# Kernel optimization log

Hardware: AMD Instinct MI355X
Metric: run time of the kernel (lower is better)

Reference implementation:

```python
import jax, jax.numpy as jnp
import numpy as np

WS = 10
NUM_HEADS = 12
DIM = 384


def setup_inputs() -> dict:
    key = jax.random.key(0)
    k1, k2, k3 = jax.random.split(key, 3)
    B, t, H, W, C = 2, 4, 44, 44, DIM
    x = jax.random.normal(k1, (B * t, H * W, C), dtype=jnp.float32)
    qkv_w = jax.random.normal(k2, (3 * C, C), dtype=jnp.float32) * 0.02
    proj_w = jax.random.normal(k3, (C, C), dtype=jnp.float32) * 0.02
    proj_b = jnp.zeros((C,), dtype=jnp.float32)
    return {"x": x, "qkv_w": qkv_w, "proj_w": proj_w, "proj_b": proj_b,
            "t": t, "H": H, "W": W}


def reference(x, qkv_w, proj_w, proj_b, t, H, W):
    ws, nh = WS, NUM_HEADS
    BT, N, C = x.shape
    B = BT // t
    hd = C // nh
    scale = hd ** (-0.5)

    ax = x.reshape(B, t, H, W, C)
    pad_r = (ws - W % ws) % ws
    pad_b = (ws - H % ws) % ws
    if pad_r > 0 or pad_b > 0:
        ax = jnp.pad(ax, ((0, 0), (0, 0), (0, pad_b), (0, pad_r), (0, 0)))
    hg, wg = (H + ws - 1) // ws, (W + ws - 1) // ws
    # partition into windows: each window holds t*ws*ws tokens
    ax = ax.reshape(B, t, hg, ws, wg, ws, C)
    ax = ax.transpose(0, 2, 4, 1, 3, 5, 6).reshape(B, hg * wg, t * ws * ws, C)

    qkv = ax @ qkv_w.T  # (B, nw, n, 3C)
    qkv = qkv.reshape(B, hg * wg, t * ws * ws, 3, nh, hd)
    qkv = qkv.transpose(3, 0, 1, 4, 2, 5)  # (3, B, nw, nh, n, hd)
    q, k, v = qkv[0], qkv[1], qkv[2]

    attn = jnp.einsum('bwhnd,bwhmd->bwhnm', q, k) * scale
    attn = jax.nn.softmax(attn, axis=-1)
    out = jnp.einsum('bwhnm,bwhmd->bwhnd', attn, v)  # (B, nw, nh, n, hd)
    out = out.transpose(0, 1, 3, 2, 4).reshape(B, hg * wg, t * ws * ws, C)

    # reverse window partition
    out = out.reshape(B, hg, wg, t, ws, ws, C)
    out = out.transpose(0, 3, 1, 4, 2, 5, 6).reshape(B, t, hg * ws, wg * ws, C)
    out = out[:, :, :H, :W, :]
    out = out.reshape(B, t * H * W, C)
    out = out @ proj_w.T + proj_b
    return out.reshape(-1, N, C)
```

## Files before the change

### kernel.cpp

```cpp
#include <hip/hip_runtime.h>
#include <cstddef>

typedef __attribute__((ext_vector_type(8))) short bf16x8;
typedef __attribute__((ext_vector_type(4))) float f32x4;
typedef __attribute__((ext_vector_type(16))) float f32x16;
typedef unsigned short ushort_t;

namespace {
constexpr int Tt = 4, Hh = 44, Ww = 44, Cc = 384, NH = 12, HD = 32;
constexpr int NWIN = 25, NT = 400, NTP = 416, NPOS = Hh * Ww;
constexpr int NTOK = 2 * Tt * NPOS;
constexpr float SCALE = 0.17677669529663687f;
constexpr float LOG2E = 1.4426950408889634f;
constexpr size_t XN  = (size_t)NTOK * Cc;
constexpr size_t WN  = (size_t)3 * Cc * Cc;
constexpr size_t PWN = (size_t)Cc * Cc;
constexpr size_t PLN = (size_t)600 * NTP * HD;
}

__device__ __forceinline__ ushort_t f2bf(float f) {
  unsigned u = __builtin_bit_cast(unsigned, f);
  u += 0x7fffu + ((u >> 16) & 1u);
  return (ushort_t)(u >> 16);
}

__device__ __forceinline__ unsigned cvt_pk_bf16(float a, float b) {
  unsigned r;
  asm volatile("v_cvt_pk_bf16_f32 %0, %1, %2" : "=v"(r) : "v"(a), "v"(b));
  return r;
}

__device__ __forceinline__ void gload16(const void* g, void* l) {
  __builtin_amdgcn_global_load_lds(
      (const __attribute__((address_space(1))) unsigned int*)g,
      (__attribute__((address_space(3))) unsigned int*)l, 16, 0, 0);
}

__global__ __launch_bounds__(256) void conv_all(
    const float* __restrict__ x, const float* __restrict__ w1,
    const float* __restrict__ w2, ushort_t* __restrict__ xo,
    ushort_t* __restrict__ w1o, ushort_t* __restrict__ w2o,
    ushort_t* __restrict__ qpl, ushort_t* __restrict__ kpl,
    ushort_t* __restrict__ vpl) {
  constexpr int XN8 = (int)(XN / 8), WN8 = (int)(WN / 8), PN8 = (int)(PWN / 8);
  constexpr int TOT8 = XN8 + WN8 + PN8;
  constexpr int ZTOT = 50 * NTP * NH;
  const int i = blockIdx.x * 256 + threadIdx.x;
  if (i < TOT8) {
    const float* s;
    ushort_t* d;
    int j;
    if (i < XN8)            { s = x;  d = xo;  j = i; }
    else if (i < XN8 + WN8) { s = w1; d = w1o; j = i - XN8; }
    else                    { s = w2; d = w2o; j = i - XN8 - WN8; }
    const float4* s4 = (const float4*)s;
    float4 a = s4[2 * j], bq = s4[2 * j + 1];
    union { bf16x8 v; ushort_t u[8]; } o;
    o.u[0] = f2bf(a.x);  o.u[1] = f2bf(a.y);  o.u[2] = f2bf(a.z);  o.u[3] = f2bf(a.w);
    o.u[4] = f2bf(bq.x); o.u[5] = f2bf(bq.y); o.u[6] = f2bf(bq.z); o.u[7] = f2bf(bq.w);
    ((bf16x8*)d)[j] = o.v;
  } else if (i < TOT8 + ZTOT) {
    const int j = i - TOT8;
    const int pair = j / NH, head = j - pair * NH;
    const int bw = pair / NTP, kk = pair - bw * NTP;
    const int win = bw % NWIN, hi5 = win / 5, wi5 = win % 5;
    bool fill;
    if (kk >= NT) {
      fill = true;
    } else {
      const int rem = kk % 100;
      const int hh = rem / 10, ww2 = rem - hh * 10;
      fill = (hi5 == 4 && hh >= 4) || (wi5 == 4 && ww2 >= 4);
    }
    if (fill) {
      const size_t off = ((size_t)(bw * NH + head) * NTP + kk) * HD;
      bf16x8 z;
      z[0]=0;z[1]=0;z[2]=0;z[3]=0;z[4]=0;z[5]=0;z[6]=0;z[7]=0;
#pragma unroll
      for (int p = 0; p < 4; ++p) {
        ((bf16x8*)(qpl + off))[p] = z;
        ((bf16x8*)(kpl + off))[p] = z;
        ((bf16x8*)(vpl + off))[p] = z;
      }
    }
  }
}

__global__ __launch_bounds__(256) void qkv_mfma(
    const ushort_t* __restrict__ xb, const ushort_t* __restrict__ wb,
    ushort_t* __restrict__ qpl, ushort_t* __restrict__ kpl,
    ushort_t* __restrict__ vpl) {
  __shared__ __align__(16) unsigned char As[8192];
  __shared__ __align__(16) unsigned char Bs[8192];
  const int nt = blockIdx.x, mt = blockIdx.y;
  const int tid = threadIdx.x, lane = tid & 63, wid = tid >> 6;
  const int wm = wid >> 1, wn = wid & 1;
  const int g = lane >> 4, q = lane & 15;
  const int m0 = mt * 128, n0 = nt * 128;

  const unsigned char* xB = (const unsigned char*)xb;
  const unsigned char* wB = (const unsigned char*)wb;

  size_t aoff[2], boff[2];
  unsigned ldsoff[2];
#pragma unroll
  for (int p = 0; p < 2; ++p) {
    const int row = wid * 32 + p * 16 + (lane >> 2);
    const int gs = (lane & 3) ^ ((row >> 1) & 3);
    aoff[p] = (size_t)(m0 + row) * 768 + gs * 16;
    boff[p] = (size_t)(n0 + row) * 768 + gs * 16;
    ldsoff[p] = wid * 2048 + p * 1024;
  }

  f32x4 acc[4][4] = {};

  for (int kb = 0; kb < 12; ++kb) {
    if (kb) __syncthreads();
#pragma unroll
    for (int p = 0; p < 2; ++p) {
      gload16(xB + aoff[p] + kb * 64, As + ldsoff[p]);
      gload16(wB + boff[p] + kb * 64, Bs + ldsoff[p]);
    }
    __syncthreads();
    bf16x8 tfr[4], wfr[4];
#pragma unroll
    for (int i = 0; i < 4; ++i) {
      const int ar = wm * 64 + i * 16 + q;
      tfr[i] = *(const bf16x8*)(As + ar * 64 + ((g ^ ((ar >> 1) & 3)) << 4));
      const int br = wn * 64 + i * 16 + q;
      wfr[i] = *(const bf16x8*)(Bs + br * 64 + ((g ^ ((br >> 1) & 3)) << 4));
    }
#pragma unroll
    for (int i = 0; i < 4; ++i)
#pragma unroll
      for (int j = 0; j < 4; ++j)
        acc[i][j] = __builtin_amdgcn_mfma_f32_16x16x32_bf16(wfr[i], tfr[j],
                                                            acc[i][j], 0, 0, 0);
  }

  const float QS = SCALE * LOG2E;
#pragma unroll
  for (int j = 0; j < 4; ++j) {
    const int t = m0 + wm * 64 + j * 16 + q;
    const int bt = t / NPOS, pos = t - bt * NPOS;
    const int h = pos / Ww, w = pos - h * Ww;
    const int b = bt >> 2, tt = bt & 3;
    const int hq = h / 10, wq = w / 10;
    const int kk = tt * 100 + (h - hq * 10) * 10 + (w - wq * 10);
    const int bw = b * NWIN + hq * 5 + wq;
#pragma unroll
    for (int i = 0; i < 4; ++i) {
      const int col = n0 + wn * 64 + i * 16 + 4 * g;
      const int which = col / Cc;
      const int head = (col - which * Cc) >> 5;
      const int d4 = col & 31;
      ushort_t* pl = which == 0 ? qpl : (which == 1 ? kpl : vpl);
      const float scl = which == 0 ? QS : 1.0f;
      uint2 st;
      st.x = cvt_pk_bf16(acc[i][j][0] * scl, acc[i][j][1] * scl);
      st.y = cvt_pk_bf16(acc[i][j][2] * scl, acc[i][j][3] * scl);
      *(uint2*)(pl + ((size_t)(bw * NH + head) * NTP + kk) * HD + d4) = st;
    }
  }
}

__global__ __launch_bounds__(512) void attn_mfma(
    const ushort_t* __restrict__ qpl, const ushort_t* __restrict__ kpl,
    const ushort_t* __restrict__ vpl, ushort_t* __restrict__ aout) {
  __shared__ __align__(16) unsigned char Vt[32 * 896];

  const int blk = blockIdx.x;
  const int strip = blk >= 600 ? 1 : 0;
  const int wh = blk - strip * 600;
  const int head = wh % NH, bw = wh / NH;
  const int b = bw / NWIN, win = bw % NWIN, hi5 = win / 5, wi5 = win % 5;

  const int tid = threadIdx.x, lane = tid & 63, wid = tid >> 6;
  const int l31 = lane & 31, hi = lane >> 5;

  const ushort_t* qbase = qpl + (size_t)wh * (NTP * HD);
  const ushort_t* kbase = kpl + (size_t)wh * (NTP * HD);
  const ushort_t* vbase = vpl + (size_t)wh * (NTP * HD);

  const int qrow = strip * 256 + wid * 32 + l31;
  const int qsrc = qrow < NTP ? qrow : NTP - 1;
  const ushort_t* qp = qbase + (size_t)qsrc * HD;
  const bf16x8 qfa = *(const bf16x8*)(qp + hi * 8);
  const bf16x8 qfb = *(const bf16x8*)(qp + 16 + hi * 8);

  unsigned koff = (unsigned)l31 * HD;
  bf16x8 kf0 = *(const bf16x8*)(kbase + koff + hi * 8);
  bf16x8 kf1 = *(const bf16x8*)(kbase + koff + 16 + hi * 8);

  for (int slot = tid; slot < 1664; slot += 512) {
    const int key = slot >> 2, dblk = (slot & 3) * 8;
    union { bf16x8 v; ushort_t u[8]; } t;
    t.v = *(const bf16x8*)(vbase + (size_t)key * HD + dblk);
    const int kc = key >> 3, klo = key & 7;
#pragma unroll
    for (int j = 0; j < 8; ++j) {
      const int d = dblk + j;
      const int f = (d & 7) ^ ((d >> 3) & 3);
      *(ushort_t*)(Vt + d * 896 + ((kc ^ f) << 4) + klo * 2) = t.u[j];
    }
  }
  __syncthreads();

  if (strip == 1 && wid >= 5) return;

  const int fv = (l31 & 7) ^ ((l31 >> 3) & 3);
  const unsigned char* vrow = Vt + l31 * 896;

  f32x16 o = {};
  float lpart = 0.f;

  for (int c = 0; c < 13; ++c) {
    f32x16 s = {};
    s = __builtin_amdgcn_mfma_f32_32x32x16_bf16(kf0, qfa, s, 0, 0, 0);
    s = __builtin_amdgcn_mfma_f32_32x32x16_bf16(kf1, qfb, s, 0, 0, 0);

    if (c < 12) {
      koff += 32u * HD;
      kf0 = *(const bf16x8*)(kbase + koff + hi * 8);
      kf1 = *(const bf16x8*)(kbase + koff + 16 + hi * 8);
    }

    if (c == 12) {
#pragma unroll
      for (int r = 8; r < 16; ++r) s[r] = -1e30f;
    }

    float e[16];
#pragma unroll
    for (int r = 0; r < 16; ++r) e[r] = __builtin_amdgcn_exp2f(s[r]);
    lpart += ((e[0] + e[1]) + (e[2] + e[3])) + ((e[4] + e[5]) + (e[6] + e[7])) +
             (((e[8] + e[9]) + (e[10] + e[11])) +
              ((e[12] + e[13]) + (e[14] + e[15])));

    unsigned w0 = cvt_pk_bf16(e[0], e[1]),   w1 = cvt_pk_bf16(e[2], e[3]);
    unsigned w2 = cvt_pk_bf16(e[4], e[5]),   w3 = cvt_pk_bf16(e[6], e[7]);
    unsigned w4 = cvt_pk_bf16(e[8], e[9]),   w5 = cvt_pk_bf16(e[10], e[11]);
    unsigned w6 = cvt_pk_bf16(e[12], e[13]), w7 = cvt_pk_bf16(e[14], e[15]);
    asm volatile("v_permlane32_swap_b32 %0, %1" : "+v"(w0), "+v"(w2));
    asm volatile("v_permlane32_swap_b32 %0, %1" : "+v"(w1), "+v"(w3));
    asm volatile("v_permlane32_swap_b32 %0, %1" : "+v"(w4), "+v"(w6));
    asm volatile("v_permlane32_swap_b32 %0, %1" : "+v"(w5), "+v"(w7));
    union { bf16x8 v; unsigned u[4]; } p0, p1;
    p0.u[0] = w0; p0.u[1] = w1; p0.u[2] = w2; p0.u[3] = w3;
    p1.u[0] = w4; p1.u[1] = w5; p1.u[2] = w6; p1.u[3] = w7;

    const bf16x8 vf0 = *(const bf16x8*)(vrow + (((4 * c + hi) ^ fv) << 4));
    const bf16x8 vf1 = *(const bf16x8*)(vrow + (((4 * c + 2 + hi) ^ fv) << 4));
    o = __builtin_amdgcn_mfma_f32_32x32x16_bf16(vf0, p0.v, o, 0, 0, 0);
    o = __builtin_amdgcn_mfma_f32_32x32x16_bf16(vf1, p1.v, o, 0, 0, 0);
  }

  lpart += __shfl_xor(lpart, 32);

  {
    const int tt = qrow / 100, rem = qrow - tt * 100;
    const int hh = rem / 10, ww2 = rem - hh * 10;
    const int h = hi5 * 10 + hh, w = wi5 * 10 + ww2;
    if (qrow < NT && h < Hh && w < Ww) {
      const int qtok = (b * Tt + tt) * NPOS + h * Ww + w;
      ushort_t* dst = aout + (size_t)qtok * Cc + head * HD;
      const float inv = 1.0f / lpart;
#pragma unroll
      for (int g4 = 0; g4 < 4; ++g4) {
        unsigned lo  = cvt_pk_bf16(o[4 * g4 + 0] * inv, o[4 * g4 + 1] * inv);
        unsigned hi2 = cvt_pk_bf16(o[4 * g4 + 2] * inv, o[4 * g4 + 3] * inv);
        uint2 st; st.x = lo; st.y = hi2;
        *(uint2*)(dst + 8 * g4 + 4 * hi) = st;
      }
    }
  }
}

__global__ __launch_bounds__(256) void proj_mfma(
    const ushort_t* __restrict__ ab, const ushort_t* __restrict__ pw,
    const float* __restrict__ bias, float* __restrict__ out) {
  __shared__ __align__(16) unsigned char As[8192];
  __shared__ __align__(16) unsigned char Bs[8192];
  const int nt = blockIdx.x, mt = blockIdx.y;
  const int tid = threadIdx.x, lane = tid & 63, wid = tid >> 6;
  const int wm = wid >> 1, wn = wid & 1;
  const int g = lane >> 4, q = lane & 15;
  const int m0 = mt * 128, n0 = nt * 128;

  const unsigned char* aB = (const unsigned char*)ab;
  const unsigned char* wB = (const unsigned char*)pw;

  size_t aoff[2], boff[2];
  unsigned ldsoff[2];
#pragma unroll
  for (int p = 0; p < 2; ++p) {
    const int row = wid * 32 + p * 16 + (lane >> 2);
    const int gs = (lane & 3) ^ ((row >> 1) & 3);
    aoff[p] = (size_t)(m0 + row) * 768 + gs * 16;
    boff[p] = (size_t)(n0 + row) * 768 + gs * 16;
    ldsoff[p] = wid * 2048 + p * 1024;
  }

  f32x4 acc[4][4] = {};

  for (int kb = 0; kb < 12; ++kb) {
    if (kb) __syncthreads();
#pragma unroll
    for (int p = 0; p < 2; ++p) {
      gload16(aB + aoff[p] + kb * 64, As + ldsoff[p]);
      gload16(wB + boff[p] + kb * 64, Bs + ldsoff[p]);
    }
    __syncthreads();
    bf16x8 tfr[4], wfr[4];
#pragma unroll
    for (int i = 0; i < 4; ++i) {
      const int ar = wm * 64 + i * 16 + q;
      tfr[i] = *(const bf16x8*)(As + ar * 64 + ((g ^ ((ar >> 1) & 3)) << 4));
      const int br = wn * 64 + i * 16 + q;
      wfr[i] = *(const bf16x8*)(Bs + br * 64 + ((g ^ ((br >> 1) & 3)) << 4));
    }
#pragma unroll
    for (int i = 0; i < 4; ++i)
#pragma unroll
      for (int j = 0; j < 4; ++j)
        acc[i][j] = __builtin_amdgcn_mfma_f32_16x16x32_bf16(wfr[i], tfr[j],
                                                            acc[i][j], 0, 0, 0);
  }

#pragma unroll
  for (int j = 0; j < 4; ++j) {
    const int t = m0 + wm * 64 + j * 16 + q;
#pragma unroll
    for (int i = 0; i < 4; ++i) {
      const int col = n0 + wn * 64 + i * 16 + 4 * g;
      const float4 bb = *(const float4*)(bias + col);
      float4 st;
      st.x = acc[i][j][0] + bb.x;
      st.y = acc[i][j][1] + bb.y;
      st.z = acc[i][j][2] + bb.z;
      st.w = acc[i][j][3] + bb.w;
      *(float4*)(out + (size_t)t * Cc + col) = st;
    }
  }
}

extern "C" void kernel_launch(void* const* d_in, const int* in_sizes, int n_in,
                              void* d_out, int out_size, void* d_ws,
                              size_t ws_size, hipStream_t stream) {
  const float* x      = (const float*)d_in[0];
  const float* qkv_w  = (const float*)d_in[1];
  const float* proj_w = (const float*)d_in[2];
  const float* proj_b = (const float*)d_in[3];

  ushort_t* xb    = (ushort_t*)d_ws;
  ushort_t* wb    = xb + XN;
  ushort_t* pwb   = wb + WN;
  ushort_t* qpl   = pwb + PWN;
  ushort_t* kpl   = qpl + PLN;
  ushort_t* vpl   = kpl + PLN;
  ushort_t* attnb = vpl + PLN;

  constexpr int TOT8 = (int)((XN + WN + PWN) / 8);
  constexpr int ZTOT = 50 * NTP * NH;
  conv_all<<<(TOT8 + ZTOT + 255) / 256, 256, 0, stream>>>(
      x, qkv_w, proj_w, xb, wb, pwb, qpl, kpl, vpl);
  qkv_mfma<<<dim3(9, 121), 256, 0, stream>>>(xb, wb, qpl, kpl, vpl);
  attn_mfma<<<1200, 512, 0, stream>>>(qpl, kpl, vpl, attnb);
  proj_mfma<<<dim3(3, 121), 256, 0, stream>>>(attnb, pwb, proj_b, (float*)d_out);
}
```

Before: 90.98 us.

## Stage QKV epilogue through LDS for coalesced stores; reorder attention blocks and set priorities

After: 101.4 us. 11.5% more time.

```diff
diff --git a/kernel.cpp b/kernel.cpp
--- a/kernel.cpp
+++ b/kernel.cpp
@@ -90,8 +90,9 @@
     const ushort_t* __restrict__ xb, const ushort_t* __restrict__ wb,
     ushort_t* __restrict__ qpl, ushort_t* __restrict__ kpl,
     ushort_t* __restrict__ vpl) {
-  __shared__ __align__(16) unsigned char As[8192];
-  __shared__ __align__(16) unsigned char Bs[8192];
+  __shared__ __align__(16) unsigned char sbuf[16384];
+  unsigned char* As = sbuf;
+  unsigned char* Bs = sbuf + 8192;
   const int nt = blockIdx.x, mt = blockIdx.y;
   const int tid = threadIdx.x, lane = tid & 63, wid = tid >> 6;
   const int wm = wid >> 1, wn = wid & 1;
@@ -138,28 +139,42 @@
                                                             acc[i][j], 0, 0, 0);
   }
 
-  const float QS = SCALE * LOG2E;
-#pragma unroll
-  for (int j = 0; j < 4; ++j) {
-    const int t = m0 + wm * 64 + j * 16 + q;
+  const float scl = (nt < 3) ? SCALE * LOG2E : 1.0f;
+  const int which = nt / 3;
+  ushort_t* pl = which == 0 ? qpl : (which == 1 ? kpl : vpl);
+  const int hbase = (nt - which * 3) * 4;
+  __syncthreads();
+#pragma unroll
+  for (int p = 0; p < 2; ++p) {
+    if (p) __syncthreads();
+    if (wm == p) {
+#pragma unroll
+      for (int j = 0; j < 4; ++j) {
+        const int tr = j * 16 + q;
+#pragma unroll
+        for (int i = 0; i < 4; ++i) {
+          const int chunk = wn * 8 + i * 2 + (g >> 1);
+          uint2 st;
+          st.x = cvt_pk_bf16(acc[i][j][0] * scl, acc[i][j][1] * scl);
+          st.y = cvt_pk_bf16(acc[i][j][2] * scl, acc[i][j][3] * scl);
+          *(uint2*)(sbuf + tr * 256 + ((chunk ^ q) << 4) + (g & 1) * 8) = st;
+        }
+      }
+    }
+    __syncthreads();
+    const int tr = tid >> 2, hl = tid & 3;
+    const int t = m0 + p * 64 + tr;
     const int bt = t / NPOS, pos = t - bt * NPOS;
     const int h = pos / Ww, w = pos - h * Ww;
     const int b = bt >> 2, tt = bt & 3;
     const int hq = h / 10, wq = w / 10;
     const int kk = tt * 100 + (h - hq * 10) * 10 + (w - wq * 10);
     const int bw = b * NWIN + hq * 5 + wq;
+    ushort_t* dst = pl + ((size_t)(bw * NH + hbase + hl) * NTP + kk) * HD;
 #pragma unroll
     for (int i = 0; i < 4; ++i) {
-      const int col = n0 + wn * 64 + i * 16 + 4 * g;
-      const int which = col / Cc;
-      const int head = (col - which * Cc) >> 5;
-      const int d4 = col & 31;
-      ushort_t* pl = which == 0 ? qpl : (which == 1 ? kpl : vpl);
-      const float scl = which == 0 ? QS : 1.0f;
-      uint2 st;
-      st.x = cvt_pk_bf16(acc[i][j][0] * scl, acc[i][j][1] * scl);
-      st.y = cvt_pk_bf16(acc[i][j][2] * scl, acc[i][j][3] * scl);
-      *(uint2*)(pl + ((size_t)(bw * NH + head) * NTP + kk) * HD + d4) = st;
+      const int cs = (hl * 4 + i) ^ (tr & 15);
+      *(bf16x8*)(dst + i * 8) = *(const bf16x8*)(sbuf + tr * 256 + (cs << 4));
     }
   }
 }
@@ -170,8 +185,8 @@
   __shared__ __align__(16) unsigned char Vt[32 * 896];
 
   const int blk = blockIdx.x;
-  const int strip = blk >= 600 ? 1 : 0;
-  const int wh = blk - strip * 600;
+  const int strip = (blk & 15) >> 3;
+  const int wh = (blk >> 4) * 8 + (blk & 7);
   const int head = wh % NH, bw = wh / NH;
   const int b = bw / NWIN, win = bw % NWIN, hi5 = win / 5, wi5 = win % 5;
 
@@ -216,8 +231,10 @@
 
   for (int c = 0; c < 13; ++c) {
     f32x16 s = {};
+    __builtin_amdgcn_s_setprio(1);
     s = __builtin_amdgcn_mfma_f32_32x32x16_bf16(kf0, qfa, s, 0, 0, 0);
     s = __builtin_amdgcn_mfma_f32_32x32x16_bf16(kf1, qfb, s, 0, 0, 0);
+    __builtin_amdgcn_s_setprio(0);
 
     if (c < 12) {
       koff += 32u * HD;
@@ -251,8 +268,10 @@
 
     const bf16x8 vf0 = *(const bf16x8*)(vrow + (((4 * c + hi) ^ fv) << 4));
     const bf16x8 vf1 = *(const bf16x8*)(vrow + (((4 * c + 2 + hi) ^ fv) << 4));
+    __builtin_amdgcn_s_setprio(1);
     o = __builtin_amdgcn_mfma_f32_32x32x16_bf16(vf0, p0.v, o, 0, 0, 0);
     o = __builtin_amdgcn_mfma_f32_32x32x16_bf16(vf1, p1.v, o, 0, 0, 0);
+    __builtin_amdgcn_s_setprio(0);
   }
 
   lpart += __shfl_xor(lpart, 32);
```
